# Optimization experiments

Measured on AMD Instinct MI355X. Metric: run time of the kernel, lower is better.

The kernel has to match this reference:

```python
import jax, jax.numpy as jnp
import numpy as np


def setup_inputs() -> dict:
    key = jax.random.key(0)
    ks = jax.random.split(key, 4)
    B, T, D, U = 64, 512, 1024, 1024
    scale = 1.0 / np.sqrt(D)
    return {
        "x": jax.random.normal(ks[0], (B, T, D), dtype=jnp.float32),
        "kernel_z": jax.random.normal(ks[1], (D, U), dtype=jnp.float32) * scale,
        "kernel_r": jax.random.normal(ks[2], (D, U), dtype=jnp.float32) * scale,
        "kernel_h": jax.random.normal(ks[3], (D, U), dtype=jnp.float32) * scale,
        "memory_z": jnp.ones((U,), dtype=jnp.float32),
        "memory_r": jnp.ones((U,), dtype=jnp.float32),
        "bias_z": jnp.zeros((U,), dtype=jnp.float32),
        "bias_r": jnp.zeros((U,), dtype=jnp.float32),
        "bias_h": jnp.zeros((U,), dtype=jnp.float32),
    }


def _bru_scan(x, kernel_z, kernel_r, kernel_h, memory_z, memory_r,
              bias_z, bias_r, bias_h):
    B, T, D = x.shape
    U = kernel_z.shape[1]
    # Precompute the three input projections for all timesteps at once
    # (same math as per-step K.dot; hoisted out of the recurrence).
    xz = jnp.einsum('btd,du->btu', x, kernel_z) + bias_z  # [B,T,U]
    xr = jnp.einsum('btd,du->btu', x, kernel_r) + bias_r
    xh = jnp.einsum('btd,du->btu', x, kernel_h) + bias_h

    def step(h, xs):
        xz_t, xr_t, xh_t = xs
        r = jnp.tanh(xr_t + h * memory_r) + 1.0
        z = jax.nn.sigmoid(xz_t + h * memory_z)
        hh = jnp.tanh(xh_t + r * h)
        out = (1.0 - z) * hh + z * h
        return out, out

    h0 = jnp.zeros((B, U), dtype=x.dtype)
    # scan over time axis
    xs = (jnp.swapaxes(xz, 0, 1), jnp.swapaxes(xr, 0, 1), jnp.swapaxes(xh, 0, 1))
    _, outs = jax.lax.scan(step, h0, xs)  # outs: [T,B,U]
    return jnp.swapaxes(outs, 0, 1)  # [B,T,U]


def reference(x, kernel_z, kernel_r, kernel_h, memory_z, memory_r,
              bias_z, bias_r, bias_h):
    return _bru_scan(x, kernel_z, kernel_r, kernel_h, memory_z, memory_r,
                     bias_z, bias_r, bias_h)
```

## Files before the change

kernel.cpp:

```cpp
#include <hip/hip_runtime.h>
#include <cmath>

using bf16x8 = __attribute__((ext_vector_type(8))) short;
using f32x4  = __attribute__((ext_vector_type(4))) float;

__device__ __forceinline__ short f2bf_rne(float f) {
    union { float f; unsigned u; } a; a.f = f;
    unsigned r = a.u + 0x7fffu + ((a.u >> 16) & 1u);
    return (short)(r >> 16);
}
__device__ __forceinline__ float bf2f(short s) {
    union { unsigned u; float f; } a;
    a.u = ((unsigned)(unsigned short)s) << 16;
    return a.f;
}
__device__ __forceinline__ void gld16(void* lds, const void* g) {
    __builtin_amdgcn_global_load_lds(
        (const __attribute__((address_space(1))) unsigned int*)g,
        (__attribute__((address_space(3))) unsigned int*)lds, 16, 0, 0);
}


__global__ __launch_bounds__(256)
void bru_conv_a(const float* __restrict__ x, short* __restrict__ Ablob,
                int T, int D, int Tc, int t0)
{
    const int gid  = blockIdx.x * 256 + threadIdx.x;
    const int blob = gid >> 10;
    const int idx  = gid & 1023;
    const int row  = idx >> 2;
    const int q    = idx & 3;
    const int mt   = blob >> 5;
    const int kt   = blob & 31;

    const int m = mt * 256 + row;
    const long xrow = (long)(m / Tc) * T + t0 + (m % Tc);
    const float* src = x + xrow * (long)D + kt * 32 + q * 8;

    float v[8];
    *(float4*)&v[0] = *(const float4*)(src);
    *(float4*)&v[4] = *(const float4*)(src + 4);

    short hi[8], lo[8];
    #pragma unroll
    for (int j = 0; j < 8; ++j) {
        hi[j] = f2bf_rne(v[j]);
        lo[j] = f2bf_rne(v[j] - bf2f(hi[j]));
    }
    short* base = Ablob + (size_t)blob * 16384 + row * 64;
    const int sh = (2 * q) ^ (row & 7);
    *(bf16x8*)(base + sh * 8)       = *(bf16x8*)hi;
    *(bf16x8*)(base + (sh ^ 1) * 8) = *(bf16x8*)lo;
}

__global__ __launch_bounds__(256)
void bru_conv_w(const float* __restrict__ wz, const float* __restrict__ wr,
                const float* __restrict__ wh, short* __restrict__ Wblob,
                int D, int U)
{
    const int gid  = blockIdx.x * 256 + threadIdx.x;
    const int blob = gid >> 10;
    const int idx  = gid & 1023;
    const int row  = idx >> 2;
    const int q    = idx & 3;

    const int g    = blob >> 7;
    const int rest = blob & 127;
    const int nt   = rest >> 5;
    const int kt   = rest & 31;

    const float* W = (g == 0) ? wz : (g == 1) ? wr : wh;
    const int d0 = kt * 32 + q * 8;
    const int u  = nt * 256 + row;

    short hi[8], lo[8];
    #pragma unroll
    for (int j = 0; j < 8; ++j) {
        float v = W[(long)(d0 + j) * U + u];
        hi[j] = f2bf_rne(v);
        lo[j] = f2bf_rne(v - bf2f(hi[j]));
    }
    short* base = Wblob + (size_t)blob * 16384 + row * 64;
    const int sh = (2 * q) ^ (row & 7);
    *(bf16x8*)(base + sh * 8)       = *(bf16x8*)hi;
    *(bf16x8*)(base + (sh ^ 1) * 8) = *(bf16x8*)lo;
}

__global__ __launch_bounds__(512, 2)
void bru_gemm_mfma(const short* __restrict__ Ablob, const short* __restrict__ Wblob,
                   const float* __restrict__ bz, const float* __restrict__ br,
                   const float* __restrict__ bh,
                   _Float16* __restrict__ proj,
                   int nmt, int U, int Mc)
{
    __shared__ char sm[131072];

    const int ngrid = gridDim.x;
    const int bid   = blockIdx.x;
    int lid = bid;
    if ((ngrid & 7) == 0) lid = (bid & 7) * (ngrid >> 3) + (bid >> 3);
    const int per_gate = nmt * 4;
    const int g  = lid / per_gate;
    const int r  = lid - g * per_gate;
    const int mt = r >> 2;
    const int nt = r & 3;

    const int tid    = threadIdx.x;
    const int w      = tid >> 6;
    const int lane   = tid & 63;
    const int wm     = w >> 2, wn = w & 3;
    const int lane15 = lane & 15;
    const int lgrp   = lane >> 4;
    const int swz    = (lane & 7) << 4;
    const int hioff  = (lgrp << 5) ^ swz;

    const char* asrc = (const char*)Ablob + (size_t)(mt * 32) * 32768;
    const char* bsrc = (const char*)Wblob + (size_t)((g * 4 + nt) * 32) * 32768;

    const int abase = wm * 16384 + lane15 * 128 + hioff;
    const int bbase = 32768 + wn * 8192 + lane15 * 128 + hioff;
    const int stoff = tid * 16;

    f32x4 acc[8][4];
    #pragma unroll
    for (int i = 0; i < 8; ++i)
        #pragma unroll
        for (int j = 0; j < 4; ++j) acc[i][j] = (f32x4)0.f;

    #pragma unroll
    for (int i = 0; i < 4; ++i) {
        gld16(sm + i * 8192 + stoff,         asrc + i * 8192 + stoff);
        gld16(sm + 32768 + i * 8192 + stoff, bsrc + i * 8192 + stoff);
    }
    asm volatile("s_waitcnt vmcnt(0)" ::: "memory");
    __builtin_amdgcn_s_barrier();

    for (int kt = 0; kt < 32; ++kt) {
        const int cb = (kt & 1) << 16;
        const int nb = cb ^ 65536;
        const char* smc = sm + cb;
        const char* abn = asrc + (size_t)(kt + 1) * 32768;
        const char* bbn = bsrc + (size_t)(kt + 1) * 32768;
        const bool pf = (kt < 31);

        bf16x8 bhf[4], blf[4];

        #pragma unroll
        for (int p = 0; p < 4; ++p) {
            const char* ap = smc + abase + p * 4096;
            bf16x8 ah0 = *(const bf16x8*)(ap);
            bf16x8 al0 = *(const bf16x8*)(smc + ((abase + p * 4096) ^ 16));
            bf16x8 ah1 = *(const bf16x8*)(ap + 2048);
            bf16x8 al1 = *(const bf16x8*)(smc + ((abase + p * 4096 + 2048) ^ 16));
            if (p == 0) {
                #pragma unroll
                for (int j = 0; j < 4; ++j) {
                    bhf[j] = *(const bf16x8*)(smc + bbase + j * 2048);
                    blf[j] = *(const bf16x8*)(smc + ((bbase + j * 2048) ^ 16));
                }
                if (pf) {
                    #pragma unroll
                    for (int i = 0; i < 4; ++i) {
                        gld16(sm + nb + i * 8192 + stoff,         abn + i * 8192 + stoff);
                        gld16(sm + nb + 32768 + i * 8192 + stoff, bbn + i * 8192 + stoff);
                    }
                }
            }
            __builtin_amdgcn_s_barrier();
            asm volatile("s_waitcnt lgkmcnt(0)" ::: "memory");
            __builtin_amdgcn_sched_barrier(0);
            __builtin_amdgcn_s_setprio(1);
            #pragma unroll
            for (int j = 0; j < 4; ++j) {
                acc[2*p  ][j] = __builtin_amdgcn_mfma_f32_16x16x32_bf16(ah0, bhf[j], acc[2*p  ][j], 0, 0, 0);
                acc[2*p  ][j] = __builtin_amdgcn_mfma_f32_16x16x32_bf16(ah0, blf[j], acc[2*p  ][j], 0, 0, 0);
                acc[2*p  ][j] = __builtin_amdgcn_mfma_f32_16x16x32_bf16(al0, bhf[j], acc[2*p  ][j], 0, 0, 0);
                acc[2*p+1][j] = __builtin_amdgcn_mfma_f32_16x16x32_bf16(ah1, bhf[j], acc[2*p+1][j], 0, 0, 0);
                acc[2*p+1][j] = __builtin_amdgcn_mfma_f32_16x16x32_bf16(ah1, blf[j], acc[2*p+1][j], 0, 0, 0);
                acc[2*p+1][j] = __builtin_amdgcn_mfma_f32_16x16x32_bf16(al1, bhf[j], acc[2*p+1][j], 0, 0, 0);
            }
            __builtin_amdgcn_s_setprio(0);
            if (p == 3) asm volatile("s_waitcnt vmcnt(0)" ::: "memory");
            __builtin_amdgcn_s_barrier();
        }
    }

    const float* bias = (g == 0) ? bz : (g == 1) ? br : bh;
    const int n0 = nt * 256 + wn * 64;
    const int m0 = mt * 256 + wm * 128;
    float bcol[4];
    #pragma unroll
    for (int j = 0; j < 4; ++j) bcol[j] = bias[n0 + j * 16 + lane15];

    _Float16* cbase = proj + (size_t)g * Mc * U;
    #pragma unroll
    for (int i = 0; i < 8; ++i) {
        #pragma unroll
        for (int jr = 0; jr < 4; ++jr) {
            const int row = m0 + i * 16 + lgrp * 4 + jr;
            _Float16* crow = cbase + (size_t)row * U + n0 + lane15;
            #pragma unroll
            for (int j = 0; j < 4; ++j)
                crow[j * 16] = (_Float16)(acc[i][j][jr] + bcol[j]);
        }
    }
}

#define PF 8
__global__ __launch_bounds__(256)
void bru_scan(const _Float16* __restrict__ proj,
              const float* __restrict__ mz, const float* __restrict__ mr,
              float* __restrict__ out,
              float* __restrict__ hstate,
              int B, int T, int U, int Tc, int t0, int Mc)
{
    const int idx = blockIdx.x * blockDim.x + threadIdx.x;
    const int b = idx / U;
    const int u = idx - b * U;

    float h = (t0 == 0) ? 0.f : hstate[idx];
    const float vmz = mz[u];
    const float vmr = mr[u];

    const _Float16* pz = proj + (long)b * Tc * U + u;
    const _Float16* pr = pz + (long)Mc * U;
    const _Float16* ph = pr + (long)Mc * U;
    float* po = out + ((long)b * T + t0) * U + u;

    _Float16 fz[PF], fr[PF], fh[PF];
    #pragma unroll
    for (int i = 0; i < PF; ++i) {
        const long o = (long)((i < Tc) ? i : (Tc - 1)) * U;
        fz[i] = pz[o]; fr[i] = pr[o]; fh[i] = ph[o];
    }

    for (int t = 0; t < Tc; t += PF) {
        #pragma unroll
        for (int i = 0; i < PF; ++i) {
            const float xz = (float)fz[i];
            const float xr = (float)fr[i];
            const float xh = (float)fh[i];
            {
                int tn = t + i + PF; if (tn > Tc - 1) tn = Tc - 1;
                const long o = (long)tn * U;
                fz[i] = pz[o]; fr[i] = pr[o]; fh[i] = ph[o];
            }
            const float e2r = __expf(2.f * (xr + h * vmr));
            const float rr  = 2.f - 2.f / (e2r + 1.f);
            const float zz  = 1.f / (1.f + __expf(-(xz + h * vmz)));
            const float e2h = __expf(2.f * (xh + rr * h));
            const float hh  = 1.f - 2.f / (e2h + 1.f);
            h = (1.f - zz) * hh + zz * h;
            if (t + i < Tc) po[(long)(t + i) * U] = h;
        }
    }
    hstate[idx] = h;
}

extern "C" void kernel_launch(void* const* d_in, const int* in_sizes, int n_in,
                              void* d_out, int out_size, void* d_ws, size_t ws_size,
                              hipStream_t stream)
{
    const float* x  = (const float*)d_in[0];
    const float* wz = (const float*)d_in[1];
    const float* wr = (const float*)d_in[2];
    const float* wh = (const float*)d_in[3];
    const float* mz = (const float*)d_in[4];
    const float* mr = (const float*)d_in[5];
    const float* bz = (const float*)d_in[6];
    const float* br = (const float*)d_in[7];
    const float* bh = (const float*)d_in[8];

    const int B = 64, T = 512, D = 1024, U = 1024;

    const size_t h_bytes = (size_t)B * U * sizeof(float);
    const size_t w_bytes = (size_t)3 * 4 * 32 * 16384 * sizeof(short);

    int Tc = T;
    while (Tc > 4) {
        const int nmt_ = B * Tc / 256;
        const size_t a_bytes_ = (size_t)nmt_ * 32 * 16384 * sizeof(short);
        const size_t p_bytes_ = 3ull * B * Tc * U * sizeof(_Float16);
        if (h_bytes + w_bytes + a_bytes_ + p_bytes_ <= ws_size) break;
        Tc >>= 1;
    }
    const int nmt = B * Tc / 256;
    const int Mc  = B * Tc;
    const size_t a_bytes = (size_t)nmt * 32 * 16384 * sizeof(short);

    float*    h_state = (float*)d_ws;
    short*    Wblob   = (short*)((char*)d_ws + h_bytes);
    short*    Ablob   = (short*)((char*)d_ws + h_bytes + w_bytes);
    _Float16* proj    = (_Float16*)((char*)d_ws + h_bytes + w_bytes + a_bytes);

    bru_conv_w<<<3 * 4 * 32 * 1024 / 256, 256, 0, stream>>>(wz, wr, wh, Wblob, D, U);

    for (int t0 = 0; t0 < T; t0 += Tc) {
        bru_conv_a<<<nmt * 32 * 1024 / 256, 256, 0, stream>>>(x, Ablob, T, D, Tc, t0);

        bru_gemm_mfma<<<3 * nmt * 4, 512, 0, stream>>>(
            Ablob, Wblob, bz, br, bh, proj, nmt, U, Mc);

        bru_scan<<<(B * U) / 256, 256, 0, stream>>>(
            proj, mz, mr, (float*)d_out, h_state, B, T, U, Tc, t0, Mc);
    }
}
```

Measured before the change: 663.7 us.

## Restructure split-bf16 GEMM: direct-to-register A loads, 32x32 MFMA, triple-buffered W

Moves the activation operand out of LDS: each wave loads its A fragments straight from global memory into registers, using a new k-major A layout written by the conversion kernel. Only the weight tile is staged in LDS, now in a three-deep ring instead of two. The MFMA shape changes from 16x16x32 to 32x32x16, tile-to-block mapping is regrouped so the gates sharing an M tile are adjacent, and the weight and A buffers are padded so prefetch can run past the last K tile. The goal is less LDS traffic and fewer barriers, at the cost of more global loads for A, higher register pressure from in-flight A fragments, and strided 16-byte writes in the A conversion kernel.

```diff
diff --git a/kernel.cpp b/kernel.cpp
--- a/kernel.cpp
+++ b/kernel.cpp
@@ -2,7 +2,7 @@
 #include <cmath>
 
 using bf16x8 = __attribute__((ext_vector_type(8))) short;
-using f32x4  = __attribute__((ext_vector_type(4))) float;
+using f32x16 = __attribute__((ext_vector_type(16))) float;
 
 __device__ __forceinline__ short f2bf_rne(float f) {
     union { float f; unsigned u; } a; a.f = f;
@@ -22,47 +22,47 @@
 
 
 __global__ __launch_bounds__(256)
-void bru_conv_a(const float* __restrict__ x, short* __restrict__ Ablob,
-                int T, int D, int Tc, int t0)
+void bru_conv_a(const float* __restrict__ x, char* __restrict__ Ablob,
+                int T, int D, int Tc, int t0, int Mc)
+{
+    const int idx = blockIdx.x * 256 + threadIdx.x;
+    const int kt = idx / Mc;
+    const int m  = idx - kt * Mc;
+
+    const long xrow = (long)(m / Tc) * T + t0 + (m % Tc);
+    const float* src = x + xrow * (long)D + kt * 32;
+
+    float v[32];
+    #pragma unroll
+    for (int i = 0; i < 8; ++i)
+        *(float4*)&v[i * 4] = *(const float4*)(src + i * 4);
+
+    #pragma unroll
+    for (int q = 0; q < 4; ++q) {
+        short hi[8], lo[8];
+        #pragma unroll
+        for (int j = 0; j < 8; ++j) {
+            float f = v[q * 8 + j];
+            hi[j] = f2bf_rne(f);
+            lo[j] = f2bf_rne(f - bf2f(hi[j]));
+        }
+        char* b0 = Ablob + ((size_t)(kt * 8 + 2 * q) * Mc + m) * 16;
+        char* b1 = Ablob + ((size_t)(kt * 8 + 2 * q + 1) * Mc + m) * 16;
+        *(bf16x8*)b0 = *(bf16x8*)hi;
+        *(bf16x8*)b1 = *(bf16x8*)lo;
+    }
+}
+
+__global__ __launch_bounds__(256)
+void bru_conv_w(const float* __restrict__ wz, const float* __restrict__ wr,
+                const float* __restrict__ wh, short* __restrict__ Wblob,
+                int D, int U)
 {
     const int gid  = blockIdx.x * 256 + threadIdx.x;
     const int blob = gid >> 10;
     const int idx  = gid & 1023;
     const int row  = idx >> 2;
     const int q    = idx & 3;
-    const int mt   = blob >> 5;
-    const int kt   = blob & 31;
-
-    const int m = mt * 256 + row;
-    const long xrow = (long)(m / Tc) * T + t0 + (m % Tc);
-    const float* src = x + xrow * (long)D + kt * 32 + q * 8;
-
-    float v[8];
-    *(float4*)&v[0] = *(const float4*)(src);
-    *(float4*)&v[4] = *(const float4*)(src + 4);
-
-    short hi[8], lo[8];
-    #pragma unroll
-    for (int j = 0; j < 8; ++j) {
-        hi[j] = f2bf_rne(v[j]);
-        lo[j] = f2bf_rne(v[j] - bf2f(hi[j]));
-    }
-    short* base = Ablob + (size_t)blob * 16384 + row * 64;
-    const int sh = (2 * q) ^ (row & 7);
-    *(bf16x8*)(base + sh * 8)       = *(bf16x8*)hi;
-    *(bf16x8*)(base + (sh ^ 1) * 8) = *(bf16x8*)lo;
-}
-
-__global__ __launch_bounds__(256)
-void bru_conv_w(const float* __restrict__ wz, const float* __restrict__ wr,
-                const float* __restrict__ wh, short* __restrict__ Wblob,
-                int D, int U)
-{
-    const int gid  = blockIdx.x * 256 + threadIdx.x;
-    const int blob = gid >> 10;
-    const int idx  = gid & 1023;
-    const int row  = idx >> 2;
-    const int q    = idx & 3;
 
     const int g    = blob >> 7;
     const int rest = blob & 127;
@@ -80,128 +80,147 @@
         hi[j] = f2bf_rne(v);
         lo[j] = f2bf_rne(v - bf2f(hi[j]));
     }
-    short* base = Wblob + (size_t)blob * 16384 + row * 64;
+    short* base = Wblob + ((size_t)((g * 4 + nt) * 34 + kt)) * 16384 + row * 64;
     const int sh = (2 * q) ^ (row & 7);
     *(bf16x8*)(base + sh * 8)       = *(bf16x8*)hi;
     *(bf16x8*)(base + (sh ^ 1) * 8) = *(bf16x8*)lo;
 }
 
 __global__ __launch_bounds__(512, 2)
-void bru_gemm_mfma(const short* __restrict__ Ablob, const short* __restrict__ Wblob,
+void bru_gemm_mfma(const char* __restrict__ Ablob, const char* __restrict__ Wblob,
                    const float* __restrict__ bz, const float* __restrict__ br,
                    const float* __restrict__ bh,
                    _Float16* __restrict__ proj,
                    int nmt, int U, int Mc)
 {
-    __shared__ char sm[131072];
+    __shared__ char sm[98304];
 
     const int ngrid = gridDim.x;
     const int bid   = blockIdx.x;
     int lid = bid;
     if ((ngrid & 7) == 0) lid = (bid & 7) * (ngrid >> 3) + (bid >> 3);
-    const int per_gate = nmt * 4;
-    const int g  = lid / per_gate;
-    const int r  = lid - g * per_gate;
-    const int mt = r >> 2;
-    const int nt = r & 3;
-
-    const int tid    = threadIdx.x;
-    const int w      = tid >> 6;
-    const int lane   = tid & 63;
-    const int wm     = w >> 2, wn = w & 3;
-    const int lane15 = lane & 15;
-    const int lgrp   = lane >> 4;
-    const int swz    = (lane & 7) << 4;
-    const int hioff  = (lgrp << 5) ^ swz;
-
-    const char* asrc = (const char*)Ablob + (size_t)(mt * 32) * 32768;
-    const char* bsrc = (const char*)Wblob + (size_t)((g * 4 + nt) * 32) * 32768;
-
-    const int abase = wm * 16384 + lane15 * 128 + hioff;
-    const int bbase = 32768 + wn * 8192 + lane15 * 128 + hioff;
-    const int stoff = tid * 16;
-
-    f32x4 acc[8][4];
-    #pragma unroll
-    for (int i = 0; i < 8; ++i)
-        #pragma unroll
-        for (int j = 0; j < 4; ++j) acc[i][j] = (f32x4)0.f;
-
-    #pragma unroll
-    for (int i = 0; i < 4; ++i) {
-        gld16(sm + i * 8192 + stoff,         asrc + i * 8192 + stoff);
-        gld16(sm + 32768 + i * 8192 + stoff, bsrc + i * 8192 + stoff);
-    }
-    asm volatile("s_waitcnt vmcnt(0)" ::: "memory");
+    const int mt  = lid / 12;
+    const int rem = lid - mt * 12;
+    const int g   = rem >> 2;
+    const int nt  = rem & 3;
+
+    const int tid  = threadIdx.x;
+    const int lane = tid & 63;
+    const int w    = tid >> 6;
+    const int wm   = w >> 1, wn = w & 1;
+    const int l31  = lane & 31;
+    const int lhi  = lane >> 5;
+
+    const char* bsrc = (const char*)Wblob + (size_t)((g * 4 + nt) * 34) * 32768;
+
+    const int arow = mt * 256 + wm * 64 + l31;
+    const size_t aMc = (size_t)Mc;
+#define AADDR(kt_, ks_, i_, lo_) \
+    (Ablob + (((size_t)((kt_) * 8 + ((ks_) * 2 + lhi) * 2 + (lo_))) * aMc + (size_t)(arow + (i_) * 32)) * 16)
+
+    const int brow = wn * 128 + l31;
+    const int br7  = brow & 7;
+#define BOFF(j_, ks_, lo_) \
+    ((size_t)(brow + (j_) * 32) * 128 + (size_t)((((((ks_) * 2 + lhi) * 2 + (lo_))) ^ br7) * 16))
+
+    f32x16 acc[2][4];
+    #pragma unroll
+    for (int i = 0; i < 2; ++i)
+        #pragma unroll
+        for (int j = 0; j < 4; ++j) acc[i][j] = (f32x16)0.f;
+
+    bf16x8 va[2][2], vb[2][2];
+
+    #pragma unroll
+    for (int i = 0; i < 4; ++i)
+        gld16(sm + i * 8192 + tid * 16, bsrc + i * 8192 + tid * 16);
+    #pragma unroll
+    for (int i = 0; i < 4; ++i)
+        gld16(sm + 32768 + i * 8192 + tid * 16, bsrc + 32768 + i * 8192 + tid * 16);
+    #pragma unroll
+    for (int i = 0; i < 2; ++i) {
+        va[i][0] = *(const bf16x8*)AADDR(0, 0, i, 0);
+        va[i][1] = *(const bf16x8*)AADDR(0, 0, i, 1);
+        vb[i][0] = *(const bf16x8*)AADDR(0, 1, i, 0);
+        vb[i][1] = *(const bf16x8*)AADDR(0, 1, i, 1);
+    }
+    __builtin_amdgcn_sched_barrier(0);
+    asm volatile("s_waitcnt vmcnt(8)" ::: "memory");
+    __builtin_amdgcn_sched_barrier(0);
     __builtin_amdgcn_s_barrier();
 
     for (int kt = 0; kt < 32; ++kt) {
-        const int cb = (kt & 1) << 16;
-        const int nb = cb ^ 65536;
-        const char* smc = sm + cb;
-        const char* abn = asrc + (size_t)(kt + 1) * 32768;
-        const char* bbn = bsrc + (size_t)(kt + 1) * 32768;
-        const bool pf = (kt < 31);
-
-        bf16x8 bhf[4], blf[4];
-
-        #pragma unroll
-        for (int p = 0; p < 4; ++p) {
-            const char* ap = smc + abase + p * 4096;
-            bf16x8 ah0 = *(const bf16x8*)(ap);
-            bf16x8 al0 = *(const bf16x8*)(smc + ((abase + p * 4096) ^ 16));
-            bf16x8 ah1 = *(const bf16x8*)(ap + 2048);
-            bf16x8 al1 = *(const bf16x8*)(smc + ((abase + p * 4096 + 2048) ^ 16));
-            if (p == 0) {
-                #pragma unroll
-                for (int j = 0; j < 4; ++j) {
-                    bhf[j] = *(const bf16x8*)(smc + bbase + j * 2048);
-                    blf[j] = *(const bf16x8*)(smc + ((bbase + j * 2048) ^ 16));
-                }
-                if (pf) {
-                    #pragma unroll
-                    for (int i = 0; i < 4; ++i) {
-                        gld16(sm + nb + i * 8192 + stoff,         abn + i * 8192 + stoff);
-                        gld16(sm + nb + 32768 + i * 8192 + stoff, bbn + i * 8192 + stoff);
-                    }
-                }
+        const char* buf  = sm + (kt % 3) * 32768;
+        char*       bufn = sm + ((kt + 2) % 3) * 32768;
+        const char* bsn  = bsrc + (size_t)(kt + 2) * 32768;
+
+        #pragma unroll
+        for (int i = 0; i < 4; ++i)
+            gld16(bufn + i * 8192 + tid * 16, bsn + i * 8192 + tid * 16);
+
+        __builtin_amdgcn_s_setprio(1);
+        #pragma unroll
+        for (int j = 0; j < 4; ++j) {
+            bf16x8 bh_ = *(const bf16x8*)(buf + BOFF(j, 0, 0));
+            bf16x8 bl_ = *(const bf16x8*)(buf + BOFF(j, 0, 1));
+            acc[0][j] = __builtin_amdgcn_mfma_f32_32x32x16_bf16(va[0][0], bh_, acc[0][j], 0, 0, 0);
+            acc[0][j] = __builtin_amdgcn_mfma_f32_32x32x16_bf16(va[0][1], bh_, acc[0][j], 0, 0, 0);
+            acc[0][j] = __builtin_amdgcn_mfma_f32_32x32x16_bf16(va[0][0], bl_, acc[0][j], 0, 0, 0);
+            acc[1][j] = __builtin_amdgcn_mfma_f32_32x32x16_bf16(va[1][0], bh_, acc[1][j], 0, 0, 0);
+            acc[1][j] = __builtin_amdgcn_mfma_f32_32x32x16_bf16(va[1][1], bh_, acc[1][j], 0, 0, 0);
+            acc[1][j] = __builtin_amdgcn_mfma_f32_32x32x16_bf16(va[1][0], bl_, acc[1][j], 0, 0, 0);
+        }
+        __builtin_amdgcn_s_setprio(0);
+
+        #pragma unroll
+        for (int i = 0; i < 2; ++i) {
+            va[i][0] = *(const bf16x8*)AADDR(kt + 1, 0, i, 0);
+            va[i][1] = *(const bf16x8*)AADDR(kt + 1, 0, i, 1);
+        }
+
+        __builtin_amdgcn_s_setprio(1);
+        #pragma unroll
+        for (int j = 0; j < 4; ++j) {
+            bf16x8 bh_ = *(const bf16x8*)(buf + BOFF(j, 1, 0));
+            bf16x8 bl_ = *(const bf16x8*)(buf + BOFF(j, 1, 1));
+            acc[0][j] = __builtin_amdgcn_mfma_f32_32x32x16_bf16(vb[0][0], bh_, acc[0][j], 0, 0, 0);
+            acc[0][j] = __builtin_amdgcn_mfma_f32_32x32x16_bf16(vb[0][1], bh_, acc[0][j], 0, 0, 0);
+            acc[0][j] = __builtin_amdgcn_mfma_f32_32x32x16_bf16(vb[0][0], bl_, acc[0][j], 0, 0, 0);
+            acc[1][j] = __builtin_amdgcn_mfma_f32_32x32x16_bf16(vb[1][0], bh_, acc[1][j], 0, 0, 0);
+            acc[1][j] = __builtin_amdgcn_mfma_f32_32x32x16_bf16(vb[1][1], bh_, acc[1][j], 0, 0, 0);
+            acc[1][j] = __builtin_amdgcn_mfma_f32_32x32x16_bf16(vb[1][0], bl_, acc[1][j], 0, 0, 0);
+        }
+        __builtin_amdgcn_s_setprio(0);
+
+        #pragma unroll
+        for (int i = 0; i < 2; ++i) {
+            vb[i][0] = *(const bf16x8*)AADDR(kt + 1, 1, i, 0);
+            vb[i][1] = *(const bf16x8*)AADDR(kt + 1, 1, i, 1);
+        }
+
+        __builtin_amdgcn_sched_barrier(0);
+        asm volatile("s_waitcnt vmcnt(8)" ::: "memory");
+        __builtin_amdgcn_sched_barrier(0);
+        __builtin_amdgcn_s_barrier();
+    }
+#undef AADDR
+#undef BOFF
+
+    const float* bias = (g == 0) ? bz : (g == 1) ? br : bh;
+    float bcol[4];
+    #pragma unroll
+    for (int j = 0; j < 4; ++j) bcol[j] = bias[nt * 256 + wn * 128 + j * 32 + l31];
+
+    _Float16* cbase = proj + (size_t)g * Mc * U + (size_t)(nt * 256 + wn * 128) + l31;
+    #pragma unroll
+    for (int i = 0; i < 2; ++i) {
+        #pragma unroll
+        for (int j = 0; j < 4; ++j) {
+            #pragma unroll
+            for (int reg = 0; reg < 16; ++reg) {
+                const int row = mt * 256 + wm * 64 + i * 32 + (reg & 3) + 8 * (reg >> 2) + 4 * lhi;
+                cbase[(size_t)row * U + j * 32] = (_Float16)(acc[i][j][reg] + bcol[j]);
             }
-            __builtin_amdgcn_s_barrier();
-            asm volatile("s_waitcnt lgkmcnt(0)" ::: "memory");
-            __builtin_amdgcn_sched_barrier(0);
-            __builtin_amdgcn_s_setprio(1);
-            #pragma unroll
-            for (int j = 0; j < 4; ++j) {
-                acc[2*p  ][j] = __builtin_amdgcn_mfma_f32_16x16x32_bf16(ah0, bhf[j], acc[2*p  ][j], 0, 0, 0);
-                acc[2*p  ][j] = __builtin_amdgcn_mfma_f32_16x16x32_bf16(ah0, blf[j], acc[2*p  ][j], 0, 0, 0);
-                acc[2*p  ][j] = __builtin_amdgcn_mfma_f32_16x16x32_bf16(al0, bhf[j], acc[2*p  ][j], 0, 0, 0);
-                acc[2*p+1][j] = __builtin_amdgcn_mfma_f32_16x16x32_bf16(ah1, bhf[j], acc[2*p+1][j], 0, 0, 0);
-                acc[2*p+1][j] = __builtin_amdgcn_mfma_f32_16x16x32_bf16(ah1, blf[j], acc[2*p+1][j], 0, 0, 0);
-                acc[2*p+1][j] = __builtin_amdgcn_mfma_f32_16x16x32_bf16(al1, bhf[j], acc[2*p+1][j], 0, 0, 0);
-            }
-            __builtin_amdgcn_s_setprio(0);
-            if (p == 3) asm volatile("s_waitcnt vmcnt(0)" ::: "memory");
-            __builtin_amdgcn_s_barrier();
-        }
-    }
-
-    const float* bias = (g == 0) ? bz : (g == 1) ? br : bh;
-    const int n0 = nt * 256 + wn * 64;
-    const int m0 = mt * 256 + wm * 128;
-    float bcol[4];
-    #pragma unroll
-    for (int j = 0; j < 4; ++j) bcol[j] = bias[n0 + j * 16 + lane15];
-
-    _Float16* cbase = proj + (size_t)g * Mc * U;
-    #pragma unroll
-    for (int i = 0; i < 8; ++i) {
-        #pragma unroll
-        for (int jr = 0; jr < 4; ++jr) {
-            const int row = m0 + i * 16 + lgrp * 4 + jr;
-            _Float16* crow = cbase + (size_t)row * U + n0 + lane15;
-            #pragma unroll
-            for (int j = 0; j < 4; ++j)
-                crow[j * 16] = (_Float16)(acc[i][j][jr] + bcol[j]);
         }
     }
 }
@@ -274,32 +293,32 @@
     const int B = 64, T = 512, D = 1024, U = 1024;
 
     const size_t h_bytes = (size_t)B * U * sizeof(float);
-    const size_t w_bytes = (size_t)3 * 4 * 32 * 16384 * sizeof(short);
+    const size_t w_bytes = (size_t)12 * 34 * 32768;
 
     int Tc = T;
     while (Tc > 4) {
-        const int nmt_ = B * Tc / 256;
-        const size_t a_bytes_ = (size_t)nmt_ * 32 * 16384 * sizeof(short);
-        const size_t p_bytes_ = 3ull * B * Tc * U * sizeof(_Float16);
+        const int Mc_ = B * Tc;
+        const size_t a_bytes_ = (size_t)33 * 8 * Mc_ * 16;
+        const size_t p_bytes_ = 3ull * Mc_ * U * sizeof(_Float16);
         if (h_bytes + w_bytes + a_bytes_ + p_bytes_ <= ws_size) break;
         Tc >>= 1;
     }
     const int nmt = B * Tc / 256;
     const int Mc  = B * Tc;
-    const size_t a_bytes = (size_t)nmt * 32 * 16384 * sizeof(short);
+    const size_t a_bytes = (size_t)33 * 8 * Mc * 16;
 
     float*    h_state = (float*)d_ws;
     short*    Wblob   = (short*)((char*)d_ws + h_bytes);
-    short*    Ablob   = (short*)((char*)d_ws + h_bytes + w_bytes);
+    char*     Ablob   = (char*)d_ws + h_bytes + w_bytes;
     _Float16* proj    = (_Float16*)((char*)d_ws + h_bytes + w_bytes + a_bytes);
 
     bru_conv_w<<<3 * 4 * 32 * 1024 / 256, 256, 0, stream>>>(wz, wr, wh, Wblob, D, U);
 
     for (int t0 = 0; t0 < T; t0 += Tc) {
-        bru_conv_a<<<nmt * 32 * 1024 / 256, 256, 0, stream>>>(x, Ablob, T, D, Tc, t0);
+        bru_conv_a<<<(Mc * 32) / 256, 256, 0, stream>>>(x, Ablob, T, D, Tc, t0, Mc);
 
         bru_gemm_mfma<<<3 * nmt * 4, 512, 0, stream>>>(
-            Ablob, Wblob, bz, br, bh, proj, nmt, U, Mc);
+            Ablob, (const char*)Wblob, bz, br, bh, proj, nmt, U, Mc);
 
         bru_scan<<<(B * U) / 256, 256, 0, stream>>>(
             proj, mz, mr, (float*)d_out, h_state, B, T, U, Tc, t0, Mc);
```

Measured after the change: 731.0 us, median of 2. 10.1% more time.
